# Performance work log

Measured on AMD Instinct MI355X. Metric: run time of the kernel, lower is better.

The kernel has to match this reference:

```python
import jax, jax.numpy as jnp
import numpy as np

C, H, G = 64, 8, 8
EPS = 1e-5


def setup_inputs() -> dict:
    key = jax.random.key(0)
    k1, k2, k3 = jax.random.split(key, 3)
    x = jax.random.normal(k1, (1, C, 16, 16, 16), dtype=jnp.float32)
    gn_weight = jnp.ones((C,), dtype=jnp.float32)
    gn_bias = jnp.zeros((C,), dtype=jnp.float32)
    qkv_w = jax.random.normal(k2, (3 * C, C), dtype=jnp.float32) * (C ** -0.5)
    out_w = jax.random.normal(k3, (C, C), dtype=jnp.float32) * (C ** -0.5)
    out_b = jnp.zeros((C,), dtype=jnp.float32)
    return {"x": x, "gn_weight": gn_weight, "gn_bias": gn_bias,
            "qkv_w": qkv_w, "out_w": out_w, "out_b": out_b}


def reference(x, gn_weight, gn_bias, qkv_w, out_w, out_b):
    B, Cc, X, Y, Z = x.shape
    D = Cc // H                     # head_dim
    S = X * Y * Z                   # flattened spatial length
    scale = D ** -0.5

    # GroupNorm over (C//G, X, Y, Z) per group
    xg = x.reshape(B, G, Cc // G, X, Y, Z)
    mu = xg.mean(axis=(2, 3, 4, 5), keepdims=True)
    var = xg.var(axis=(2, 3, 4, 5), keepdims=True)
    xn = ((xg - mu) * jax.lax.rsqrt(var + EPS)).reshape(B, Cc, X, Y, Z)
    xn = xn * gn_weight[None, :, None, None, None] + gn_bias[None, :, None, None, None]

    # 1x1x1 conv == channel matmul
    qkv = jnp.einsum('oc,bcxyz->boxyz', qkv_w, xn)
    q, k, v = jnp.split(qkv, 3, axis=1)            # each [B, C, X, Y, Z]
    q = q.reshape(B, H, D, S)
    k = k.reshape(B, H, D, S)
    v = v.reshape(B, H, D, S)

    scores = jnp.einsum('bhds,bhdt->bhst', q, k) * scale   # [B,H,S,S]
    probs = jax.nn.softmax(scores, axis=-1)
    out = jnp.einsum('bhst,bhdt->bhds', probs, v)          # [B,H,D,S]
    out = out.reshape(B, Cc, X, Y, Z)

    out = jnp.einsum('oc,bcxyz->boxyz', out_w, out) + out_b[None, :, None, None, None]
    return out + x
```

## Files before the change

### kernel.cpp

```cpp
#include <hip/hip_runtime.h>
#include <math.h>

#define S 4096
#define EPS 1e-5f

#define WS_PSUM 0
#define WS_PSQ  64
#define WS_ATT  16384
#define QT_B 1310720
#define KT_B 1835008
#define VB_B 2359296

typedef _Float16 h8_t __attribute__((ext_vector_type(8)));
typedef __fp16   fp16v2 __attribute__((ext_vector_type(2)));
typedef float    f4_t  __attribute__((ext_vector_type(4)));
typedef float    f16_t __attribute__((ext_vector_type(16)));

union H8 { h8_t h; int4 v; int i[4]; };

static __device__ __forceinline__ int pkrtz(float a, float b) {
    fp16v2 p = __builtin_amdgcn_cvt_pkrtz(a, b);
    union { fp16v2 h; int i; } u; u.h = p; return u.i;
}

#define EXP2_BITS(x) ((int)fmaf((x), 1024.0f, 15316.0f))

__global__ __launch_bounds__(256) void k_gnstat1(const float* __restrict__ x,
                                                 float* __restrict__ ws) {
    int b = blockIdx.x;
    int tid = threadIdx.x;
    const float4* p = (const float4*)(x + b * 4096);
    float s = 0.f, sq = 0.f;
    #pragma unroll
    for (int i = 0; i < 4; ++i) {
        float4 v = p[tid + i * 256];
        s  += v.x + v.y + v.z + v.w;
        sq += v.x * v.x + v.y * v.y + v.z * v.z + v.w * v.w;
    }
    #pragma unroll
    for (int m = 32; m >= 1; m >>= 1) {
        s  += __shfl_xor(s, m);
        sq += __shfl_xor(sq, m);
    }
    __shared__ float ls[4], lq[4];
    int w = tid >> 6;
    if ((tid & 63) == 0) { ls[w] = s; lq[w] = sq; }
    __syncthreads();
    if (tid == 0) {
        ws[WS_PSUM + b] = ls[0] + ls[1] + ls[2] + ls[3];
        ws[WS_PSQ  + b] = lq[0] + lq[1] + lq[2] + lq[3];
    }
}

__global__ __launch_bounds__(256) void k_qkv(const float* __restrict__ x,
                                             const float* __restrict__ qkvw,
                                             const float* __restrict__ gnw,
                                             const float* __restrict__ gnb,
                                             float* __restrict__ ws) {
    __shared__ float la[64], lb2[64], lw[256], lbias[4];
    int tid = threadIdx.x;
    int o0 = blockIdx.y * 4;
    int s = blockIdx.x * 256 + tid;

    if (tid < 64) {
        float sm = ws[WS_PSUM + tid];
        float sq = ws[WS_PSQ + tid];
        #pragma unroll
        for (int m = 1; m < 8; m <<= 1) {
            sm += __shfl_xor(sm, m);
            sq += __shfl_xor(sq, m);
        }
        const float inv_n = 1.0f / 32768.0f;
        float mu  = sm * inv_n;
        float var = sq * inv_n - mu * mu;
        float rs  = rsqrtf(var + EPS);
        float a   = rs * gnw[tid];
        la[tid]  = a;
        lb2[tid] = gnb[tid] - mu * a;
    }
    __syncthreads();
    lw[tid] = qkvw[o0 * 64 + tid] * la[tid & 63];
    {
        int wv = tid >> 6, ln = tid & 63;
        float pb = qkvw[(o0 + wv) * 64 + ln] * lb2[ln];
        #pragma unroll
        for (int m = 1; m < 64; m <<= 1) pb += __shfl_xor(pb, m);
        if (ln == 0) lbias[wv] = pb;
    }
    __syncthreads();

    float acc[4];
    #pragma unroll
    for (int o = 0; o < 4; ++o) acc[o] = lbias[o];
    for (int c = 0; c < 64; ++c) {
        float xv = x[c * S + s];
        #pragma unroll
        for (int o = 0; o < 4; ++o) acc[o] = fmaf(lw[o * 64 + c], xv, acc[o]);
    }

    char* base = (char*)ws;
    if (o0 < 64) {
        const float qsc = 0.51006776f;
        int hh = o0 >> 3, db = o0 & 7;
        int2 r;
        r.x = pkrtz(acc[0] * qsc, acc[1] * qsc);
        r.y = pkrtz(acc[2] * qsc, acc[3] * qsc);
        *(int2*)(base + QT_B + (size_t)(hh * 4096 + s) * 16 + db * 2) = r;
    } else if (o0 < 128) {
        int hh = (o0 - 64) >> 3, db = o0 & 7;
        int2 r;
        r.x = pkrtz(acc[0], acc[1]);
        r.y = pkrtz(acc[2], acc[3]);
        *(int2*)(base + KT_B + (size_t)(hh * 4096 + s) * 16 + db * 2) = r;
    } else {
        int hh = (o0 - 128) >> 3, db = o0 & 7;
        _Float16* vb = (_Float16*)(base + VB_B);
        #pragma unroll
        for (int d = 0; d < 4; ++d)
            vb[(size_t)((hh * 8 + db + d) * 4096) + s] = (_Float16)acc[d];
    }
}

__global__ __launch_bounds__(512, 4) void k_attn(float* __restrict__ ws) {
    const int h = blockIdx.y;
    const int q0 = blockIdx.x * 32;
    const int tid = threadIdx.x;
    const int w = tid >> 6;
    const int lane = tid & 63;
    const int col16 = lane & 15;
    const int quad = lane >> 4;
    const int col32 = lane & 31;
    const int half = lane >> 5;

    const char* base = (const char*)ws;
    const _Float16* Qt = (const _Float16*)(base + QT_B) + (size_t)h * 4096 * 8;
    const _Float16* Kt = (const _Float16*)(base + KT_B) + (size_t)h * 4096 * 8;
    const _Float16* Vb = (const _Float16*)(base + VB_B) + (size_t)h * 8 * 4096;

    __shared__ __align__(16) char smem[20480 + 14336];
    _Float16* Pw = (_Float16*)smem + (size_t)w * 1280;
    f4_t* red = (f4_t*)(smem + 20480);

    H8 qf;
    qf.i[0] = qf.i[1] = qf.i[2] = qf.i[3] = 0;
    if (half == 0) qf.v = *(const int4*)(Qt + (size_t)(q0 + col32) * 8);

    H8 kf;
    kf.i[0] = kf.i[1] = kf.i[2] = kf.i[3] = 0;
    H8 vf;
    {
        int c8 = (col16 == 8) ? 0x3C003C00 : 0;
        vf.i[0] = c8; vf.i[1] = c8; vf.i[2] = c8; vf.i[3] = c8;
    }

    const int tbase = w * 512;
    if (half == 0) kf.v = *(const int4*)(Kt + (size_t)(tbase + col32) * 8);

    f4_t acc0 = {0.f, 0.f, 0.f, 0.f};
    f4_t acc1 = {0.f, 0.f, 0.f, 0.f};
    f16_t zc = {0.f, 0.f, 0.f, 0.f, 0.f, 0.f, 0.f, 0.f,
                0.f, 0.f, 0.f, 0.f, 0.f, 0.f, 0.f, 0.f};

    for (int it = 0; it < 16; ++it) {
        const int tt = tbase + it * 32;
        if (col16 < 8)
            vf.v = *(const int4*)(Vb + (size_t)col16 * 4096 + tt + quad * 8);

        f16_t sc = __builtin_amdgcn_mfma_f32_32x32x16_f16(kf.h, qf.h, zc, 0, 0, 0);

        H8 nk = kf;
        if (half == 0)
            nk.v = *(const int4*)(Kt + (size_t)(tt + 32 + col32) * 8);

        #pragma unroll
        for (int b = 0; b < 4; ++b) {
            int i0 = EXP2_BITS(sc[4 * b + 0]);
            int i1 = EXP2_BITS(sc[4 * b + 1]);
            int i2 = EXP2_BITS(sc[4 * b + 2]);
            int i3 = EXP2_BITS(sc[4 * b + 3]);
            int2 wv = { i0 | (i1 << 16), i2 | (i3 << 16) };
            *(int2*)(Pw + col32 * 40 + 8 * b + 4 * half) = wv;
        }

        H8 p0, p1;
        p0.v = *(const int4*)(Pw + col16 * 40 + quad * 8);
        p1.v = *(const int4*)(Pw + (col16 + 16) * 40 + quad * 8);

        acc0 = __builtin_amdgcn_mfma_f32_16x16x32_f16(vf.h, p0.h, acc0, 0, 0, 0);
        acc1 = __builtin_amdgcn_mfma_f32_16x16x32_f16(vf.h, p1.h, acc1, 0, 0, 0);

        kf = nk;
    }

    __syncthreads();
    if (w > 0) {
        red[((w - 1) * 2 + 0) * 64 + lane] = acc0;
        red[((w - 1) * 2 + 1) * 64 + lane] = acc1;
    }
    __syncthreads();
    if (w == 0) {
        #pragma unroll
        for (int r = 0; r < 7; ++r) {
            acc0 += red[(r * 2 + 0) * 64 + lane];
            acc1 += red[(r * 2 + 1) * 64 + lane];
        }
        float inv0 = 1.0f / __shfl(acc0[0], 32 + col16, 64);
        float inv1 = 1.0f / __shfl(acc1[0], 32 + col16, 64);
        if (quad < 2) {
            float* att = ws + WS_ATT + (size_t)(h * 8 + quad * 4) * S + q0;
            #pragma unroll
            for (int r = 0; r < 4; ++r) {
                att[r * S + col16]      = acc0[r] * inv0;
                att[r * S + 16 + col16] = acc1[r] * inv1;
            }
        }
    }
}

__global__ __launch_bounds__(256) void k_out(const float* __restrict__ x,
                                             const float* __restrict__ outw,
                                             const float* __restrict__ outb,
                                             const float* __restrict__ ws,
                                             float* __restrict__ out) {
    __shared__ float lw[64];
    int tid = threadIdx.x;
    int o = blockIdx.y;
    int s = blockIdx.x * 256 + tid;
    if (tid < 64) lw[tid] = outw[o * 64 + tid];
    __syncthreads();

    float acc = outb[o];
    const float* att = ws + WS_ATT;
    for (int c = 0; c < 64; ++c)
        acc = fmaf(lw[c], att[c * S + s], acc);
    out[o * S + s] = acc + x[o * S + s];
}

extern "C" void kernel_launch(void* const* d_in, const int* in_sizes, int n_in,
                              void* d_out, int out_size, void* d_ws, size_t ws_size,
                              hipStream_t stream) {
    const float* x    = (const float*)d_in[0];
    const float* gnw  = (const float*)d_in[1];
    const float* gnb  = (const float*)d_in[2];
    const float* qkvw = (const float*)d_in[3];
    const float* outw = (const float*)d_in[4];
    const float* outb = (const float*)d_in[5];
    float* out = (float*)d_out;
    float* ws  = (float*)d_ws;

    hipLaunchKernelGGL(k_gnstat1, dim3(64), dim3(256), 0, stream, x, ws);
    hipLaunchKernelGGL(k_qkv, dim3(16, 48), dim3(256), 0, stream, x, qkvw, gnw, gnb, ws);
    hipLaunchKernelGGL(k_attn, dim3(128, 8), dim3(512), 0, stream, ws);
    hipLaunchKernelGGL(k_out, dim3(16, 64), dim3(256), 0, stream, x, outw, outb, ws, out);
}
```

Before: 93.03 us.

## Software-pipeline attention loop with double-buffered P tiles and V prefetch

Restructures the attention inner loop so the PV MFMAs for the previous tile run while the current tile's QK scores are being exponentiated. P is double-buffered in LDS, and V is prefetched one iteration ahead. This is meant to hide MFMA and LDS latency behind the exp/pack work. It grows LDS to 40KB per block, which can cut occupancy, and adds register pressure from the extra V fragments.

```diff
diff --git a/kernel.cpp b/kernel.cpp
--- a/kernel.cpp
+++ b/kernel.cpp
@@ -137,9 +137,10 @@
     const _Float16* Kt = (const _Float16*)(base + KT_B) + (size_t)h * 4096 * 8;
     const _Float16* Vb = (const _Float16*)(base + VB_B) + (size_t)h * 8 * 4096;
 
-    __shared__ __align__(16) char smem[20480 + 14336];
-    _Float16* Pw = (_Float16*)smem + (size_t)w * 1280;
-    f4_t* red = (f4_t*)(smem + 20480);
+    __shared__ __align__(16) char smem[40960];
+    _Float16* Pb0 = (_Float16*)smem + (size_t)w * 2560;
+    _Float16* Pb1 = Pb0 + 1280;
+    f4_t* red = (f4_t*)smem;
 
     H8 qf;
     qf.i[0] = qf.i[1] = qf.i[2] = qf.i[3] = 0;
@@ -147,31 +148,27 @@
 
     H8 kf;
     kf.i[0] = kf.i[1] = kf.i[2] = kf.i[3] = 0;
-    H8 vf;
+    H8 vf, vprev;
     {
         int c8 = (col16 == 8) ? 0x3C003C00 : 0;
         vf.i[0] = c8; vf.i[1] = c8; vf.i[2] = c8; vf.i[3] = c8;
     }
+    vprev = vf;
 
     const int tbase = w * 512;
     if (half == 0) kf.v = *(const int4*)(Kt + (size_t)(tbase + col32) * 8);
+    if (col16 < 8) vf.v = *(const int4*)(Vb + (size_t)col16 * 4096 + tbase + quad * 8);
 
     f4_t acc0 = {0.f, 0.f, 0.f, 0.f};
     f4_t acc1 = {0.f, 0.f, 0.f, 0.f};
     f16_t zc = {0.f, 0.f, 0.f, 0.f, 0.f, 0.f, 0.f, 0.f,
                 0.f, 0.f, 0.f, 0.f, 0.f, 0.f, 0.f, 0.f};
 
-    for (int it = 0; it < 16; ++it) {
-        const int tt = tbase + it * 32;
-        if (col16 < 8)
-            vf.v = *(const int4*)(Vb + (size_t)col16 * 4096 + tt + quad * 8);
-
+    {
         f16_t sc = __builtin_amdgcn_mfma_f32_32x32x16_f16(kf.h, qf.h, zc, 0, 0, 0);
-
-        H8 nk = kf;
-        if (half == 0)
-            nk.v = *(const int4*)(Kt + (size_t)(tt + 32 + col32) * 8);
-
+        H8 nk = kf, nv = vf;
+        if (half == 0) nk.v = *(const int4*)(Kt + (size_t)(tbase + 32 + col32) * 8);
+        if (col16 < 8) nv.v = *(const int4*)(Vb + (size_t)col16 * 4096 + tbase + 32 + quad * 8);
         #pragma unroll
         for (int b = 0; b < 4; ++b) {
             int i0 = EXP2_BITS(sc[4 * b + 0]);
@@ -179,17 +176,47 @@
             int i2 = EXP2_BITS(sc[4 * b + 2]);
             int i3 = EXP2_BITS(sc[4 * b + 3]);
             int2 wv = { i0 | (i1 << 16), i2 | (i3 << 16) };
-            *(int2*)(Pw + col32 * 40 + 8 * b + 4 * half) = wv;
-        }
+            *(int2*)(Pb0 + col32 * 40 + 8 * b + 4 * half) = wv;
+        }
+        vprev = vf; kf = nk; vf = nv;
+    }
+
+    for (int it = 1; it < 16; ++it) {
+        const int tt = tbase + it * 32;
+        _Float16* Pcur  = (it & 1) ? Pb1 : Pb0;
+        _Float16* Pprev = (it & 1) ? Pb0 : Pb1;
+
+        f16_t sc = __builtin_amdgcn_mfma_f32_32x32x16_f16(kf.h, qf.h, zc, 0, 0, 0);
+
+        H8 nk = kf, nv = vf;
+        if (half == 0) nk.v = *(const int4*)(Kt + (size_t)(tt + 32 + col32) * 8);
+        if (col16 < 8) nv.v = *(const int4*)(Vb + (size_t)col16 * 4096 + tt + 32 + quad * 8);
 
         H8 p0, p1;
-        p0.v = *(const int4*)(Pw + col16 * 40 + quad * 8);
-        p1.v = *(const int4*)(Pw + (col16 + 16) * 40 + quad * 8);
-
-        acc0 = __builtin_amdgcn_mfma_f32_16x16x32_f16(vf.h, p0.h, acc0, 0, 0, 0);
-        acc1 = __builtin_amdgcn_mfma_f32_16x16x32_f16(vf.h, p1.h, acc1, 0, 0, 0);
-
-        kf = nk;
+        p0.v = *(const int4*)(Pprev + col16 * 40 + quad * 8);
+        p1.v = *(const int4*)(Pprev + (col16 + 16) * 40 + quad * 8);
+        acc0 = __builtin_amdgcn_mfma_f32_16x16x32_f16(vprev.h, p0.h, acc0, 0, 0, 0);
+        acc1 = __builtin_amdgcn_mfma_f32_16x16x32_f16(vprev.h, p1.h, acc1, 0, 0, 0);
+
+        #pragma unroll
+        for (int b = 0; b < 4; ++b) {
+            int i0 = EXP2_BITS(sc[4 * b + 0]);
+            int i1 = EXP2_BITS(sc[4 * b + 1]);
+            int i2 = EXP2_BITS(sc[4 * b + 2]);
+            int i3 = EXP2_BITS(sc[4 * b + 3]);
+            int2 wv = { i0 | (i1 << 16), i2 | (i3 << 16) };
+            *(int2*)(Pcur + col32 * 40 + 8 * b + 4 * half) = wv;
+        }
+
+        vprev = vf; kf = nk; vf = nv;
+    }
+
+    {
+        H8 p0, p1;
+        p0.v = *(const int4*)(Pb1 + col16 * 40 + quad * 8);
+        p1.v = *(const int4*)(Pb1 + (col16 + 16) * 40 + quad * 8);
+        acc0 = __builtin_amdgcn_mfma_f32_16x16x32_f16(vprev.h, p0.h, acc0, 0, 0, 0);
+        acc1 = __builtin_amdgcn_mfma_f32_16x16x32_f16(vprev.h, p1.h, acc1, 0, 0, 0);
     }
 
     __syncthreads();
```

Result: no change. 93.49 us (+0.5%).
